# Kernel optimization log

Measured on AMD Instinct MI355X. Metric: run time of the kernel, lower is better.

## Reference

```python
import jax, jax.numpy as jnp
import numpy as np

NUM_EXPERTS = 8
TOP_K = 2
B, S, H = 4, 1024, 1024
FF = 2 * H  # expert hidden = 2*hidden_size per the torch code


def setup_inputs() -> dict:
    key = jax.random.key(0)
    ks = jax.random.split(key, 5)
    scale = 0.02
    return {
        "x": jax.random.normal(ks[0], (B, S, H), dtype=jnp.float32),
        "Wg": jax.random.normal(ks[1], (H, NUM_EXPERTS), dtype=jnp.float32) * scale,
        "bg": jnp.zeros((NUM_EXPERTS,), dtype=jnp.float32),
        "W1": jax.random.normal(ks[2], (NUM_EXPERTS, H, FF), dtype=jnp.float32) * scale,
        "b1": jnp.zeros((NUM_EXPERTS, FF), dtype=jnp.float32),
        "W2": jax.random.normal(ks[3], (NUM_EXPERTS, FF, H), dtype=jnp.float32) * scale,
        "b2": jnp.zeros((NUM_EXPERTS, H), dtype=jnp.float32),
    }


def reference(x, Wg, bg, W1, b1, W2, b2):
    b, s, h = x.shape
    xf = x.reshape(-1, h)  # [T, H]
    # Gating: softmax over experts, then top-k and renormalize (as in torch code)
    gate_scores = jax.nn.softmax(xf @ Wg + bg, axis=-1)  # [T, E]
    top_v, top_i = jax.lax.top_k(gate_scores, TOP_K)      # [T, K]
    top_v = top_v / jnp.sum(top_v, axis=-1, keepdims=True)
    # Combine weights per (token, expert): gate if expert selected else 0
    combine = jnp.sum(jax.nn.one_hot(top_i, NUM_EXPERTS, dtype=xf.dtype)
                      * top_v[..., None], axis=1)         # [T, E]
    # Dense all-expert MLP (eval-mode dropout = identity), then gated combine
    hmid = jax.nn.relu(jnp.einsum('th,ehf->tef', xf, W1) + b1)  # [T, E, FF]
    yexp = jnp.einsum('tef,efh->teh', hmid, W2) + b2            # [T, E, H]
    out = jnp.einsum('te,teh->th', combine, yexp)               # [T, H]
    return out.reshape(b, s, h)
```

## Files before the change

kernel.cpp:

```cpp
#include <hip/hip_runtime.h>
#include <hip/hip_bf16.h>

#define T_TOK 4096
#define HD    1024
#define FFD   2048
#define NE    8
#define TWMAX 71

typedef __attribute__((ext_vector_type(8))) short short8;
typedef __attribute__((ext_vector_type(4))) float f32x4;

__device__ __forceinline__ unsigned short f2bf(float f) {
  __hip_bfloat16 h = __float2bfloat16(f);
  return __builtin_bit_cast(unsigned short, h);
}

__device__ __forceinline__ void gload_lds16(const unsigned short* g, unsigned short* l) {
  __builtin_amdgcn_global_load_lds(
      (const __attribute__((address_space(1))) unsigned int*)g,
      (__attribute__((address_space(3))) unsigned int*)l, 16, 0, 0);
}

__device__ __forceinline__ bool decode_tile(const int* __restrict__ counts,
                                            int j, int& e, int& rt, int& row0) {
  int acc = 0, base = 0;
#pragma unroll
  for (int k = 0; k < NE; ++k) {
    int nt = (counts[k] + 127) >> 7;
    if (j < acc + nt) { e = k; rt = j - acc; row0 = base + (rt << 7); return true; }
    acc += nt; base += nt << 7;
  }
  return false;
}

__global__ __launch_bounds__(256) void gate_kernel(
    const float* __restrict__ x, const float* __restrict__ Wg,
    const float* __restrict__ bg,
    int* __restrict__ top_i, float2* __restrict__ top_w,
    unsigned short* __restrict__ xbf, float* __restrict__ out)
{
  {
    size_t b = ((size_t)blockIdx.x * 256 + threadIdx.x) * 16;
    float4 z = make_float4(0.f, 0.f, 0.f, 0.f);
#pragma unroll
    for (int q = 0; q < 4; ++q) *(float4*)(out + b + q * 4) = z;
  }

  const int wave = threadIdx.x >> 6;
  const int lane = threadIdx.x & 63;
  const int t = blockIdx.x * 4 + wave;
  if (t >= T_TOK) return;

  float acc[NE];
#pragma unroll
  for (int e = 0; e < NE; ++e) acc[e] = 0.f;

  const float* xr = x + (size_t)t * HD;
  unsigned short* xo = xbf + (size_t)t * HD;
#pragma unroll
  for (int it = 0; it < 4; ++it) {
    const int h0 = lane * 4 + it * 256;
    float4 xv = *(const float4*)(xr + h0);
#pragma unroll
    for (int j = 0; j < 4; ++j) {
      float xs = (&xv.x)[j];
      float4 a = *(const float4*)(Wg + (size_t)(h0 + j) * NE);
      float4 b = *(const float4*)(Wg + (size_t)(h0 + j) * NE + 4);
      acc[0] = fmaf(xs, a.x, acc[0]); acc[1] = fmaf(xs, a.y, acc[1]);
      acc[2] = fmaf(xs, a.z, acc[2]); acc[3] = fmaf(xs, a.w, acc[3]);
      acc[4] = fmaf(xs, b.x, acc[4]); acc[5] = fmaf(xs, b.y, acc[5]);
      acc[6] = fmaf(xs, b.z, acc[6]); acc[7] = fmaf(xs, b.w, acc[7]);
    }
    ushort4 u;
    u.x = f2bf(xv.x); u.y = f2bf(xv.y); u.z = f2bf(xv.z); u.w = f2bf(xv.w);
    *(ushort4*)(xo + h0) = u;
  }
#pragma unroll
  for (int off = 32; off > 0; off >>= 1) {
#pragma unroll
    for (int e = 0; e < NE; ++e) acc[e] += __shfl_xor(acc[e], off);
  }
  if (lane == 0) {
    float lg[NE];
#pragma unroll
    for (int e = 0; e < NE; ++e) lg[e] = acc[e] + bg[e];
    int i1 = 0;
#pragma unroll
    for (int e = 1; e < NE; ++e) if (lg[e] > lg[i1]) i1 = e;
    int i2 = (i1 == 0) ? 1 : 0;
#pragma unroll
    for (int e = 0; e < NE; ++e) if (e != i1 && lg[e] > lg[i2]) i2 = e;
    float p2 = expf(lg[i2] - lg[i1]);
    float s  = 1.f + p2;
    top_i[t] = i1 | (i2 << 8);
    top_w[t] = make_float2(1.f / s, p2 / s);
  }
}

__global__ __launch_bounds__(256) void route_kernel(
    const int* __restrict__ top_i, const float2* __restrict__ top_w,
    int* __restrict__ counts, int* __restrict__ ids, float* __restrict__ wts)
{
  const int e   = blockIdx.x;
  const int tid = threadIdx.x;
  __shared__ int psum[256];

  const int t0 = tid * 16;
  unsigned int flags = 0;
  int cnt = 0;
#pragma unroll
  for (int j = 0; j < 16; ++j) {
    int ti = top_i[t0 + j];
    bool m = ((ti & 255) == e) || (((ti >> 8) & 255) == e);
    flags |= (m ? 1u : 0u) << j;
    cnt += m;
  }
  psum[tid] = cnt;
  __syncthreads();
  for (int off = 1; off < 256; off <<= 1) {
    int v = (tid >= off) ? psum[tid - off] : 0;
    __syncthreads();
    psum[tid] += v;
    __syncthreads();
  }
  int rank = psum[tid] - cnt;
#pragma unroll
  for (int j = 0; j < 16; ++j) {
    if (flags & (1u << j)) {
      int t = t0 + j;
      int ti = top_i[t];
      float2 w = top_w[t];
      ids[e * T_TOK + rank] = t;
      wts[e * T_TOK + rank] = ((ti & 255) == e) ? w.x : w.y;
      ++rank;
    }
  }
  if (tid == 255) counts[e] = psum[255];
}

__global__ __launch_bounds__(256) void transpose_cvt_kernel(
    const float* __restrict__ in, unsigned short* __restrict__ out,
    int R, int C)
{
  __shared__ float tile[64][69];
  const int z  = blockIdx.z;
  const int r0 = blockIdx.y * 64, c0 = blockIdx.x * 64;
  const int t  = threadIdx.x;
  const float* ip = in + ((size_t)z * R + r0) * C + c0;
  int tr = t >> 4, tc = (t & 15) * 4;
#pragma unroll
  for (int j = 0; j < 4; ++j) {
    float4 v = *(const float4*)(ip + (size_t)(tr + j * 16) * C + tc);
    float* tp = &tile[tr + j * 16][tc];
    tp[0] = v.x; tp[1] = v.y; tp[2] = v.z; tp[3] = v.w;
  }
  __syncthreads();
  unsigned short* op = out + ((size_t)z * C + c0) * R + r0;
  int oc = t >> 4, orr = (t & 15) * 4;
#pragma unroll
  for (int j = 0; j < 4; ++j) {
    int c = oc + j * 16;
    ushort4 w;
    w.x = f2bf(tile[orr + 0][c]);
    w.y = f2bf(tile[orr + 1][c]);
    w.z = f2bf(tile[orr + 2][c]);
    w.w = f2bf(tile[orr + 3][c]);
    *(ushort4*)(op + (size_t)c * R + orr) = w;
  }
}

template<int KD, int ND, bool G1M, bool GATHER_A>
__global__ __launch_bounds__(256, 3) void pair_gemm128_kernel(
    const unsigned short* __restrict__ A,
    const unsigned short* __restrict__ BT,
    const float* __restrict__ bias,
    const int* __restrict__ counts, const int* __restrict__ ids,
    const float* __restrict__ wts,
    unsigned short* __restrict__ Hout, float* __restrict__ out)
{
  int e, rt, row0;
  if (!decode_tile(counts, blockIdx.y, e, rt, row0)) return;
  const int ct  = blockIdx.x;
  const int cnt = counts[e];

  __shared__ __align__(16) unsigned short As[128 * 64];
  __shared__ __align__(16) unsigned short Bs[128 * 64];

  const int tid  = threadIdx.x;
  const int w    = tid >> 6;
  const int lane = tid & 63;
  const int g    = lane >> 4;
  const int rA   = lane & 15;
  const int wr   = w >> 1;
  const int wc   = w & 1;
  const int sw   = rA & 7;
  const int srow = lane >> 3;
  const int lc8  = ((lane & 7) ^ srow) * 8;

  const unsigned short* arow[4];
#pragma unroll
  for (int jj = 0; jj < 4; ++jj) {
    const int lrow = w * 32 + jj * 8 + srow;
    int src;
    if constexpr (GATHER_A) {
      int i = rt * 128 + lrow;
      src = ids[e * T_TOK + (i < cnt ? i : cnt - 1)];
    } else {
      src = row0 + lrow;
    }
    arow[jj] = A + (size_t)src * KD + lc8;
  }
  const unsigned short* Bb = BT + ((size_t)e * ND + (size_t)ct * 128) * KD + lc8;

  f32x4 acc[4][4];
#pragma unroll
  for (int mf = 0; mf < 4; ++mf)
#pragma unroll
    for (int nf = 0; nf < 4; ++nf)
      acc[mf][nf] = (f32x4){0.f, 0.f, 0.f, 0.f};

  for (int kc = 0; kc < KD; kc += 64) {
    __syncthreads();
#pragma unroll
    for (int jj = 0; jj < 4; ++jj) {
      const int rg = w * 32 + jj * 8;
      gload_lds16(arow[jj] + kc, &As[rg * 64]);
      gload_lds16(Bb + (size_t)(rg + srow) * KD + kc, &Bs[rg * 64]);
    }
    __syncthreads();
#pragma unroll
    for (int ks = 0; ks < 2; ++ks) {
      const int pc = ((ks * 4 + g) ^ sw) << 3;
      short8 af[4], bf[4];
#pragma unroll
      for (int mf = 0; mf < 4; ++mf)
        af[mf] = *(const short8*)&As[(wr * 64 + mf * 16 + rA) * 64 + pc];
#pragma unroll
      for (int nf = 0; nf < 4; ++nf)
        bf[nf] = *(const short8*)&Bs[(wc * 64 + nf * 16 + rA) * 64 + pc];
#pragma unroll
      for (int mf = 0; mf < 4; ++mf)
#pragma unroll
        for (int nf = 0; nf < 4; ++nf)
          acc[mf][nf] = __builtin_amdgcn_mfma_f32_16x16x32_bf16(
              af[mf], bf[nf], acc[mf][nf], 0, 0, 0);
    }
  }

  float bv[4];
#pragma unroll
  for (int nf = 0; nf < 4; ++nf)
    bv[nf] = bias[e * ND + ct * 128 + wc * 64 + nf * 16 + rA];

  if constexpr (G1M) {
#pragma unroll
    for (int mf = 0; mf < 4; ++mf)
#pragma unroll
      for (int r = 0; r < 4; ++r) {
        const int row = row0 + wr * 64 + mf * 16 + g * 4 + r;
        unsigned short* hrow = Hout + (size_t)row * FFD + ct * 128 + wc * 64 + rA;
#pragma unroll
        for (int nf = 0; nf < 4; ++nf)
          hrow[nf * 16] = f2bf(fmaxf(acc[mf][nf][r] + bv[nf], 0.f));
      }
  } else {
#pragma unroll
    for (int mf = 0; mf < 4; ++mf)
#pragma unroll
      for (int r = 0; r < 4; ++r) {
        const int i = rt * 128 + wr * 64 + mf * 16 + g * 4 + r;
        if (i >= cnt) continue;
        const int tok = ids[e * T_TOK + i];
        const float wt = wts[e * T_TOK + i];
        float* orow = out + (size_t)tok * HD + ct * 128 + wc * 64 + rA;
#pragma unroll
        for (int nf = 0; nf < 4; ++nf)
          atomicAdd(&orow[nf * 16], wt * (acc[mf][nf][r] + bv[nf]));
      }
  }
}

extern "C" void kernel_launch(void* const* d_in, const int* in_sizes, int n_in,
                              void* d_out, int out_size, void* d_ws, size_t ws_size,
                              hipStream_t stream) {
  const float* x  = (const float*)d_in[0];
  const float* Wg = (const float*)d_in[1];
  const float* bg = (const float*)d_in[2];
  const float* W1 = (const float*)d_in[3];
  const float* b1 = (const float*)d_in[4];
  const float* W2 = (const float*)d_in[5];
  const float* b2 = (const float*)d_in[6];
  float* out = (float*)d_out;

  const size_t OFF_TOPI = 512;
  const size_t OFF_TOPW = OFF_TOPI + (size_t)T_TOK * 4;
  const size_t OFF_IDS  = OFF_TOPW + (size_t)T_TOK * 8;
  const size_t OFF_WTS  = OFF_IDS + (size_t)T_TOK * NE * 4;
  const size_t OFF_XBF  = OFF_WTS + (size_t)T_TOK * NE * 4;
  const size_t OFF_WT   = OFF_XBF + (size_t)T_TOK * HD * 2;
  const size_t OFF_H    = OFF_WT + (size_t)NE * HD * FFD * 2;
  const size_t REQ      = OFF_H + (size_t)9216 * FFD * 2;

  if (ws_size < REQ) return;

  int*            counts = (int*)d_ws;
  int*            top_i  = (int*)((char*)d_ws + OFF_TOPI);
  float2*         top_w  = (float2*)((char*)d_ws + OFF_TOPW);
  int*            ids    = (int*)((char*)d_ws + OFF_IDS);
  float*          wts    = (float*)((char*)d_ws + OFF_WTS);
  unsigned short* xbf    = (unsigned short*)((char*)d_ws + OFF_XBF);
  unsigned short* WT     = (unsigned short*)((char*)d_ws + OFF_WT);
  unsigned short* H      = (unsigned short*)((char*)d_ws + OFF_H);

  gate_kernel<<<T_TOK / 4, 256, 0, stream>>>(x, Wg, bg, top_i, top_w, xbf, out);
  route_kernel<<<NE, 256, 0, stream>>>(top_i, top_w, counts, ids, wts);

  transpose_cvt_kernel<<<dim3(FFD / 64, HD / 64, NE), 256, 0, stream>>>(W1, WT, HD, FFD);
  pair_gemm128_kernel<HD, FFD, true, true><<<dim3(FFD / 128, TWMAX), 256, 0, stream>>>(
      xbf, WT, b1, counts, ids, wts, H, nullptr);

  transpose_cvt_kernel<<<dim3(HD / 64, FFD / 64, NE), 256, 0, stream>>>(W2, WT, FFD, HD);
  pair_gemm128_kernel<FFD, HD, false, false><<<dim3(HD / 128, TWMAX), 256, 0, stream>>>(
      H, WT, b2, counts, ids, wts, nullptr, out);
}
```

Baseline: 190.5 us.

## Double-buffer expert GEMM LDS tiles and enlarge tiles for first GEMM

Generalizes the grouped expert GEMM into a templated kernel with double-buffered LDS staging, so the next K-chunk's global-to-LDS loads overlap the current chunk's MFMA work and each iteration needs only one barrier. The first GEMM moves to 256x256 tiles with 8 waves and the second keeps 128x128. Blocks are mapped expert-major via blockIdx.x with 256-row padding per expert, which grows the H workspace. Larger tiles cut redundant operand loads but lower occupancy and waste more work on padded rows.

New measurement: 224.4 us. 1.18x slower.

```diff
diff --git a/kernel.cpp b/kernel.cpp
--- a/kernel.cpp
+++ b/kernel.cpp
@@ -5,7 +5,6 @@
 #define HD    1024
 #define FFD   2048
 #define NE    8
-#define TWMAX 71
 
 typedef __attribute__((ext_vector_type(8))) short short8;
 typedef __attribute__((ext_vector_type(4))) float f32x4;
@@ -19,18 +18,6 @@
   __builtin_amdgcn_global_load_lds(
       (const __attribute__((address_space(1))) unsigned int*)g,
       (__attribute__((address_space(3))) unsigned int*)l, 16, 0, 0);
-}
-
-__device__ __forceinline__ bool decode_tile(const int* __restrict__ counts,
-                                            int j, int& e, int& rt, int& row0) {
-  int acc = 0, base = 0;
-#pragma unroll
-  for (int k = 0; k < NE; ++k) {
-    int nt = (counts[k] + 127) >> 7;
-    if (j < acc + nt) { e = k; rt = j - acc; row0 = base + (rt << 7); return true; }
-    acc += nt; base += nt << 7;
-  }
-  return false;
 }
 
 __global__ __launch_bounds__(256) void gate_kernel(
@@ -169,8 +156,8 @@
   }
 }
 
-template<int KD, int ND, bool G1M, bool GATHER_A>
-__global__ __launch_bounds__(256, 3) void pair_gemm128_kernel(
+template<int KD, int ND, int BM, int BN, int WM, int WN, bool G1M, bool GATHER_A>
+__global__ __launch_bounds__(WM * WN * 64, 2) void pair_gemm_kernel(
     const unsigned short* __restrict__ A,
     const unsigned short* __restrict__ BT,
     const float* __restrict__ bias,
@@ -178,103 +165,139 @@
     const float* __restrict__ wts,
     unsigned short* __restrict__ Hout, float* __restrict__ out)
 {
-  int e, rt, row0;
-  if (!decode_tile(counts, blockIdx.y, e, rt, row0)) return;
-  const int ct  = blockIdx.x;
-  const int cnt = counts[e];
-
-  __shared__ __align__(16) unsigned short As[128 * 64];
-  __shared__ __align__(16) unsigned short Bs[128 * 64];
+  constexpr int W   = WM * WN;
+  constexpr int MF  = BM / WM / 16;
+  constexpr int NF  = BN / WN / 16;
+  constexpr int JA  = BM / (8 * W);
+  constexpr int JB  = BN / (8 * W);
+  constexpr int NT  = KD / 64;
+  constexpr int CT  = ND / BN;
+  constexpr int WMS = BM / WM;
+  constexpr int WNS = BN / WN;
+
+  const int e    = blockIdx.x & 7;
+  const int slot = blockIdx.x >> 3;
+  int cnt = 0, base = 0;
+#pragma unroll
+  for (int k = 0; k < NE; ++k) {
+    int c = counts[k];
+    if (k < e)  base += (c + 255) & ~255;
+    if (k == e) cnt = c;
+  }
+  const int ntiles = (cnt + BM - 1) / BM;
+  if (slot >= ntiles * CT) return;
+  const int rt   = slot % ntiles;
+  const int ct   = slot / ntiles;
+  const int row0 = base + rt * BM;
+
+  __shared__ __align__(16) unsigned short As[2][BM * 64];
+  __shared__ __align__(16) unsigned short Bs[2][BN * 64];
 
   const int tid  = threadIdx.x;
   const int w    = tid >> 6;
   const int lane = tid & 63;
   const int g    = lane >> 4;
   const int rA   = lane & 15;
-  const int wr   = w >> 1;
-  const int wc   = w & 1;
+  const int wr   = w / WN;
+  const int wc   = w % WN;
   const int sw   = rA & 7;
   const int srow = lane >> 3;
   const int lc8  = ((lane & 7) ^ srow) * 8;
 
-  const unsigned short* arow[4];
-#pragma unroll
-  for (int jj = 0; jj < 4; ++jj) {
-    const int lrow = w * 32 + jj * 8 + srow;
+  const unsigned short* aptr[JA];
+#pragma unroll
+  for (int jj = 0; jj < JA; ++jj) {
+    const int lrow = (w * JA + jj) * 8 + srow;
     int src;
     if constexpr (GATHER_A) {
-      int i = rt * 128 + lrow;
+      int i = rt * BM + lrow;
       src = ids[e * T_TOK + (i < cnt ? i : cnt - 1)];
     } else {
       src = row0 + lrow;
     }
-    arow[jj] = A + (size_t)src * KD + lc8;
-  }
-  const unsigned short* Bb = BT + ((size_t)e * ND + (size_t)ct * 128) * KD + lc8;
-
-  f32x4 acc[4][4];
-#pragma unroll
-  for (int mf = 0; mf < 4; ++mf)
-#pragma unroll
-    for (int nf = 0; nf < 4; ++nf)
+    aptr[jj] = A + (size_t)src * KD + lc8;
+  }
+  const unsigned short* bptr[JB];
+#pragma unroll
+  for (int jj = 0; jj < JB; ++jj) {
+    const int lrow = (w * JB + jj) * 8 + srow;
+    bptr[jj] = BT + ((size_t)e * ND + ct * BN + lrow) * KD + lc8;
+  }
+
+  f32x4 acc[MF][NF];
+#pragma unroll
+  for (int mf = 0; mf < MF; ++mf)
+#pragma unroll
+    for (int nf = 0; nf < NF; ++nf)
       acc[mf][nf] = (f32x4){0.f, 0.f, 0.f, 0.f};
 
-  for (int kc = 0; kc < KD; kc += 64) {
-    __syncthreads();
-#pragma unroll
-    for (int jj = 0; jj < 4; ++jj) {
-      const int rg = w * 32 + jj * 8;
-      gload_lds16(arow[jj] + kc, &As[rg * 64]);
-      gload_lds16(Bb + (size_t)(rg + srow) * KD + kc, &Bs[rg * 64]);
-    }
-    __syncthreads();
+  auto stage = [&](int buf, int kc) {
+#pragma unroll
+    for (int jj = 0; jj < JA; ++jj)
+      gload_lds16(aptr[jj] + kc, &As[buf][(w * JA + jj) * 8 * 64]);
+#pragma unroll
+    for (int jj = 0; jj < JB; ++jj)
+      gload_lds16(bptr[jj] + kc, &Bs[buf][(w * JB + jj) * 8 * 64]);
+  };
+
+  stage(0, 0);
+  __syncthreads();
+
+#pragma unroll 2
+  for (int t = 0; t < NT; ++t) {
+    const int cur = t & 1;
+    if (t + 1 < NT) stage(cur ^ 1, (t + 1) * 64);
+    __builtin_amdgcn_sched_barrier(0);
 #pragma unroll
     for (int ks = 0; ks < 2; ++ks) {
       const int pc = ((ks * 4 + g) ^ sw) << 3;
-      short8 af[4], bf[4];
-#pragma unroll
-      for (int mf = 0; mf < 4; ++mf)
-        af[mf] = *(const short8*)&As[(wr * 64 + mf * 16 + rA) * 64 + pc];
-#pragma unroll
-      for (int nf = 0; nf < 4; ++nf)
-        bf[nf] = *(const short8*)&Bs[(wc * 64 + nf * 16 + rA) * 64 + pc];
-#pragma unroll
-      for (int mf = 0; mf < 4; ++mf)
-#pragma unroll
-        for (int nf = 0; nf < 4; ++nf)
+      short8 bf[NF];
+#pragma unroll
+      for (int nf = 0; nf < NF; ++nf)
+        bf[nf] = *(const short8*)&Bs[cur][(wc * WNS + nf * 16 + rA) * 64 + pc];
+#pragma unroll
+      for (int mf = 0; mf < MF; ++mf) {
+        short8 af = *(const short8*)&As[cur][(wr * WMS + mf * 16 + rA) * 64 + pc];
+#pragma unroll
+        for (int nf = 0; nf < NF; ++nf)
           acc[mf][nf] = __builtin_amdgcn_mfma_f32_16x16x32_bf16(
-              af[mf], bf[nf], acc[mf][nf], 0, 0, 0);
+              af, bf[nf], acc[mf][nf], 0, 0, 0);
+      }
     }
-  }
-
-  float bv[4];
-#pragma unroll
-  for (int nf = 0; nf < 4; ++nf)
-    bv[nf] = bias[e * ND + ct * 128 + wc * 64 + nf * 16 + rA];
+    asm volatile("s_waitcnt vmcnt(0)" ::: "memory");
+    __builtin_amdgcn_sched_barrier(0);
+    __builtin_amdgcn_s_barrier();
+    __builtin_amdgcn_sched_barrier(0);
+  }
+
+  float bv[NF];
+#pragma unroll
+  for (int nf = 0; nf < NF; ++nf)
+    bv[nf] = bias[e * ND + ct * BN + wc * WNS + nf * 16 + rA];
 
   if constexpr (G1M) {
 #pragma unroll
-    for (int mf = 0; mf < 4; ++mf)
+    for (int mf = 0; mf < MF; ++mf)
 #pragma unroll
       for (int r = 0; r < 4; ++r) {
-        const int row = row0 + wr * 64 + mf * 16 + g * 4 + r;
-        unsigned short* hrow = Hout + (size_t)row * FFD + ct * 128 + wc * 64 + rA;
-#pragma unroll
-        for (int nf = 0; nf < 4; ++nf)
+        const int row = row0 + wr * WMS + mf * 16 + g * 4 + r;
+        unsigned short* hrow = Hout + (size_t)row * FFD + ct * BN + wc * WNS + rA;
+#pragma unroll
+        for (int nf = 0; nf < NF; ++nf)
           hrow[nf * 16] = f2bf(fmaxf(acc[mf][nf][r] + bv[nf], 0.f));
       }
   } else {
 #pragma unroll
-    for (int mf = 0; mf < 4; ++mf)
+    for (int mf = 0; mf < MF; ++mf)
 #pragma unroll
       for (int r = 0; r < 4; ++r) {
-        const int i = rt * 128 + wr * 64 + mf * 16 + g * 4 + r;
+        const int i = rt * BM + wr * WMS + mf * 16 + g * 4 + r;
         if (i >= cnt) continue;
         const int tok = ids[e * T_TOK + i];
         const float wt = wts[e * T_TOK + i];
-        float* orow = out + (size_t)tok * HD + ct * 128 + wc * 64 + rA;
-#pragma unroll
-        for (int nf = 0; nf < 4; ++nf)
+        float* orow = out + (size_t)tok * HD + ct * BN + wc * WNS + rA;
+#pragma unroll
+        for (int nf = 0; nf < NF; ++nf)
           atomicAdd(&orow[nf * 16], wt * (acc[mf][nf][r] + bv[nf]));
       }
   }
@@ -299,7 +322,7 @@
   const size_t OFF_XBF  = OFF_WTS + (size_t)T_TOK * NE * 4;
   const size_t OFF_WT   = OFF_XBF + (size_t)T_TOK * HD * 2;
   const size_t OFF_H    = OFF_WT + (size_t)NE * HD * FFD * 2;
-  const size_t REQ      = OFF_H + (size_t)9216 * FFD * 2;
+  const size_t REQ      = OFF_H + (size_t)10240 * FFD * 2;
 
   if (ws_size < REQ) return;
 
@@ -316,10 +339,10 @@
   route_kernel<<<NE, 256, 0, stream>>>(top_i, top_w, counts, ids, wts);
 
   transpose_cvt_kernel<<<dim3(FFD / 64, HD / 64, NE), 256, 0, stream>>>(W1, WT, HD, FFD);
-  pair_gemm128_kernel<HD, FFD, true, true><<<dim3(FFD / 128, TWMAX), 256, 0, stream>>>(
-      xbf, WT, b1, counts, ids, wts, H, nullptr);
+  pair_gemm_kernel<HD, FFD, 256, 256, 2, 4, true, true>
+      <<<NE * 128, 512, 0, stream>>>(xbf, WT, b1, counts, ids, wts, H, nullptr);
 
   transpose_cvt_kernel<<<dim3(HD / 64, FFD / 64, NE), 256, 0, stream>>>(W2, WT, FFD, HD);
-  pair_gemm128_kernel<FFD, HD, false, false><<<dim3(HD / 128, TWMAX), 256, 0, stream>>>(
-      H, WT, b2, counts, ids, wts, nullptr, out);
-}
+  pair_gemm_kernel<FFD, HD, 128, 128, 2, 2, false, false>
+      <<<NE * 256, 256, 0, stream>>>(H, WT, b2, counts, ids, wts, nullptr, out);
+}
```
